# Performance work log

Measured on AMD Instinct MI355X. Metric: run time of the kernel, lower is better.

Reference implementation:

```python
import jax, jax.numpy as jnp
import numpy as np

H = 16      # n_heads
DK = 64     # d_k = d_v = input_dim // n_heads
D = 1024    # input_dim = ouput_dim


def setup_inputs() -> dict:
    key = jax.random.key(0)
    ks = jax.random.split(key, 10)
    s = 1.0 / np.float32(np.sqrt(D))
    inp = {
        'X':  jax.random.normal(ks[0], (2048, D), jnp.float32),
        'X1': jax.random.normal(ks[1], (3072, D), jnp.float32),
        'WQ':  jax.random.normal(ks[2], (D, H * DK), jnp.float32) * s,
        'WK':  jax.random.normal(ks[3], (D, H * DK), jnp.float32) * s,
        'WV':  jax.random.normal(ks[4], (D, H * DK), jnp.float32) * s,
        'WQ1': jax.random.normal(ks[5], (D, H * DK), jnp.float32) * s,
        'WK1': jax.random.normal(ks[6], (D, H * DK), jnp.float32) * s,
        'WV1': jax.random.normal(ks[7], (D, H * DK), jnp.float32) * s,
        'Wfc':  jax.random.normal(ks[8], (H * DK, D), jnp.float32) * s,
        'Wfc1': jax.random.normal(ks[9], (H * DK, D), jnp.float32) * s,
    }
    return inp


def _heads(x):
    # [N, H*DK] -> [H, N, DK]  (matches .view(-1,H,DK).transpose(0,1))
    return x.reshape(-1, H, DK).transpose(1, 0, 2)


def reference(X, X1, WQ, WK, WV, WQ1, WK1, WV1, Wfc, Wfc1):
    scale = jnp.float32(1.0 / np.sqrt(DK))
    Q,  K,  V  = _heads(X @ WQ),  _heads(X @ WK),  _heads(X @ WV)   # [H,N,DK]
    Q1, K1, V1 = _heads(X1 @ WQ1), _heads(X1 @ WK1), _heads(X1 @ WV1)  # [H,N1,DK]

    # direction 1: queries from X1 attend over X
    scores = jnp.einsum('hqd,hkd->hqk', Q1, K) * scale           # [H,N1,N]
    attn = jax.nn.softmax(scores, axis=-1)
    context = jnp.einsum('hqk,hkd->hqd', attn, V)                # [H,N1,DK]

    # direction 2: queries from X attend over X1
    scores1 = jnp.einsum('hqd,hkd->hqk', Q, K1) * scale          # [H,N,N1]
    attn1 = jax.nn.softmax(scores1, axis=-1)
    context1 = jnp.einsum('hqk,hkd->hqd', attn1, V1)             # [H,N,DK]

    # faithful to torch: .transpose(1,2).reshape(-1, H*DK) (head/len axes interleaved)
    context = context.transpose(0, 2, 1).reshape(-1, H * DK)     # [N1, H*DK] rows
    context1 = context1.transpose(0, 2, 1).reshape(-1, H * DK)   # [N,  H*DK] rows

    output = context @ Wfc     # [N1, D]
    output1 = context1 @ Wfc1  # [N,  D]
    return (output, output1)
```

## Files before the change

### kernel.cpp

```cpp
#include <hip/hip_runtime.h>
#include <stdint.h>

typedef unsigned short u16;
typedef unsigned int u32;
typedef u16   u16x4  __attribute__((ext_vector_type(4)));
typedef u16   u16x8  __attribute__((ext_vector_type(8)));
typedef __bf16 bf16x8 __attribute__((ext_vector_type(8)));
typedef float f32x4  __attribute__((ext_vector_type(4)));
typedef u32   u32x2  __attribute__((ext_vector_type(2)));
typedef u32   u32x4  __attribute__((ext_vector_type(4)));

typedef __attribute__((address_space(3))) u16 lds_u16;
typedef __attribute__((address_space(1))) const u16 glb_u16;

static __device__ __forceinline__ u16 f32_bf16(float f) {
    uint32_t u = __builtin_bit_cast(uint32_t, f);
    u += 0x7fffu + ((u >> 16) & 1u);
    return (u16)(u >> 16);
}
static __device__ __forceinline__ u32 pack2(float a, float b) {
#if __has_builtin(__builtin_amdgcn_perm)
    u32 ua = __builtin_bit_cast(u32, a) + 0x8000u;
    u32 ub = __builtin_bit_cast(u32, b) + 0x8000u;
    return __builtin_amdgcn_perm(ub, ua, 0x07060302u);
#else
    return (u32)f32_bf16(a) | ((u32)f32_bf16(b) << 16);
#endif
}
#if __has_builtin(__builtin_amdgcn_exp2f)
#define EXP2(x) __builtin_amdgcn_exp2f(x)
#else
#define EXP2(x) __expf((x) * 0.69314718056f)
#endif
static __device__ __forceinline__ u16x8 cvt8(f32x4 a, f32x4 b) {
    u16x8 v;
#pragma unroll
    for (int e = 0; e < 4; ++e) { v[e] = f32_bf16(a[e]); v[4 + e] = f32_bf16(b[e]); }
    return v;
}

__global__ __launch_bounds__(256) void detect_k(const u16* __restrict__ X, uint32_t* flag) {
    __shared__ int cnt[256];
    int t = threadIdx.x;
    int c = 0;
#pragma unroll
    for (int i = 0; i < 4; ++i) {
        u16 v = X[t + 256 * i];
        int e = (v >> 7) & 0xFF;
        c += (e >= 0xC2) ? 1 : 0;
    }
    cnt[t] = c;
    __syncthreads();
    for (int s = 128; s > 0; s >>= 1) {
        if (t < s) cnt[t] += cnt[t + s];
        __syncthreads();
    }
    if (t == 0) *flag = (cnt[0] > 32) ? 1u : 0u;
}

struct XJob { const void* in; u16* out; int n; };

__global__ __launch_bounds__(256) void convert_x(XJob j0, XJob j1, const uint32_t* __restrict__ flag) {
    const XJob job = (blockIdx.y == 0) ? j0 : j1;
    const bool f32in = (*flag != 0u);
    const int stride = gridDim.x * 256 * 8;
    for (int i = ((int)blockIdx.x * 256 + (int)threadIdx.x) * 8; i < job.n; i += stride) {
        u16x8 v;
        if (f32in) {
            const float* p = (const float*)job.in + i;
            v = cvt8(*(const f32x4*)p, *(const f32x4*)(p + 4));
        } else {
            v = *(const u16x8*)((const u16*)job.in + i);
        }
        *(u16x8*)(job.out + i) = v;
    }
}

struct WJob { const void* in; u16* out; };
struct WBatch8 { WJob j[8]; };

__global__ __launch_bounds__(256) void convert_w(WBatch8 args, const uint32_t* __restrict__ flag) {
    __shared__ u16 tile[64][72];
    const bool f32in = (*flag != 0u);
    const void* in = args.j[blockIdx.z].in;
    u16*       out = args.j[blockIdx.z].out;
    const int t  = threadIdx.x;
    const int r0 = blockIdx.y * 64, c0 = blockIdx.x * 64;
    const int lr = t >> 3, lc = (t & 7) * 8;
#pragma unroll
    for (int pass = 0; pass < 2; ++pass) {
        int r = lr + pass * 32;
        u16x8 v;
        if (f32in) {
            const float* p = (const float*)in + (size_t)(r0 + r) * 1024 + c0 + lc;
            v = cvt8(*(const f32x4*)p, *(const f32x4*)(p + 4));
        } else {
            v = *(const u16x8*)((const u16*)in + (size_t)(r0 + r) * 1024 + c0 + lc);
        }
#pragma unroll
        for (int e = 0; e < 8; ++e) tile[r][lc + e] = v[e];
    }
    __syncthreads();
#pragma unroll
    for (int pass = 0; pass < 2; ++pass) {
        int n = lr + pass * 32;
        u16x8 v;
#pragma unroll
        for (int e = 0; e < 8; ++e) v[e] = tile[lc + e][n];
        *(u16x8*)(out + (size_t)(c0 + n) * 1024 + r0 + lc) = v;
    }
}

struct GemmJob  { const u16* A; const u16* Bt; void* C; int M; int cF32able; int cOffElems; int vtNk; float cScale; };
struct GemmBatch6 { GemmJob j[6]; };

__global__ __launch_bounds__(256) void gemm_bt(GemmBatch6 b, const uint32_t* __restrict__ flag) {
    const GemmJob job = b.j[blockIdx.z];
    const int K = 1024, N = 1024;
    const int m0 = blockIdx.x * 128;
    if (m0 >= job.M) return;
    const int n0 = blockIdx.y * 128;
    const bool cF = job.cF32able && (*flag != 0u);

    __shared__ u16 As[128 * 64];
    __shared__ u16 Bs[128 * 64];

    const int tid  = threadIdx.x;
    const int lane = tid & 63, wave = tid >> 6;
    const int quad = lane >> 4, l16 = lane & 15;
    const int wrow = wave >> 1, wcol = wave & 1;

    f32x4 acc[4][4];
#pragma unroll
    for (int i = 0; i < 4; ++i)
#pragma unroll
        for (int j = 0; j < 4; ++j) acc[i][j] = (f32x4){0.f, 0.f, 0.f, 0.f};

    for (int k0 = 0; k0 < K; k0 += 64) {
        __syncthreads();
#pragma unroll
        for (int i = 0; i < 4; ++i) {
            int id = tid + 256 * i;
            int row = id >> 3, slot = id & 7;
            int src = (slot ^ (row & 7)) * 8;
            __builtin_amdgcn_global_load_lds(
                (glb_u16*)(job.A + (size_t)(m0 + row) * K + k0 + src),
                (lds_u16*)(As + (size_t)id * 8), 16, 0, 0);
            __builtin_amdgcn_global_load_lds(
                (glb_u16*)(job.Bt + (size_t)(n0 + row) * K + k0 + src),
                (lds_u16*)(Bs + (size_t)id * 8), 16, 0, 0);
        }
        __syncthreads();

#pragma unroll
        for (int kc2 = 0; kc2 < 2; ++kc2) {
            bf16x8 af[4], bfb[4];
#pragma unroll
            for (int i = 0; i < 4; ++i) {
                int r  = wrow * 64 + i * 16 + l16;
                af[i]  = *(const bf16x8*)(As + r * 64 + (((kc2 * 4 + quad) ^ (r & 7)) * 8));
                int rn = wcol * 64 + i * 16 + l16;
                bfb[i] = *(const bf16x8*)(Bs + rn * 64 + (((kc2 * 4 + quad) ^ (rn & 7)) * 8));
            }
#pragma unroll
            for (int i = 0; i < 4; ++i)
#pragma unroll
                for (int j = 0; j < 4; ++j)
                    acc[i][j] = __builtin_amdgcn_mfma_f32_16x16x32_bf16(af[i], bfb[j], acc[i][j], 0, 0, 0);
        }
    }

    if (job.vtNk > 0) {
        u16* VT = (u16*)job.C;
        const int Nk2 = job.vtNk;
#pragma unroll
        for (int i = 0; i < 4; ++i)
#pragma unroll
            for (int j = 0; j < 4; ++j) {
                int n   = n0 + wcol * 64 + j * 16 + l16;
                int hh  = n >> 6, dd = n & 63;
                int key = m0 + wrow * 64 + i * 16 + quad * 4;
                int bq  = key & 31;
                int kp  = (key & ~31) | (((bq >> 2) & 3) * 8 + (bq >> 4) * 4);
                u16x4 vv;
#pragma unroll
                for (int r = 0; r < 4; ++r) vv[r] = f32_bf16(acc[i][j][r]);
                *(u16x4*)(VT + (size_t)hh * 64 * Nk2 + (size_t)dd * Nk2 + kp) = vv;
            }
    } else if (cF) {
        float* C = (float*)job.C + job.cOffElems;
#pragma unroll
        for (int i = 0; i < 4; ++i)
#pragma unroll
            for (int j = 0; j < 4; ++j)
#pragma unroll
                for (int r = 0; r < 4; ++r) {
                    int gr = m0 + wrow * 64 + i * 16 + quad * 4 + r;
                    int gc = n0 + wcol * 64 + j * 16 + l16;
                    C[(size_t)gr * N + gc] = acc[i][j][r];
                }
    } else {
        u16* C = (u16*)job.C + job.cOffElems;
        const float cs = job.cScale;
#pragma unroll
        for (int i = 0; i < 4; ++i)
#pragma unroll
            for (int j = 0; j < 4; ++j)
#pragma unroll
                for (int r = 0; r < 4; ++r) {
                    int gr = m0 + wrow * 64 + i * 16 + quad * 4 + r;
                    int gc = n0 + wcol * 64 + j * 16 + l16;
                    C[(size_t)gr * N + gc] = f32_bf16(acc[i][j][r] * cs);
                }
    }
}

struct AttnDir { const u16* Q; const u16* K; const u16* VT; u16* ctxT; int Nq; int Nk; int nBlk; };

__global__ __launch_bounds__(256, 4) void attn_k(AttnDir d0, AttnDir d1) {
    const int D = 1024;
    int b = blockIdx.x;
    const AttnDir dd = (b < d0.nBlk) ? d0 : d1;
    if (blockIdx.x >= (unsigned)d0.nBlk) b -= d0.nBlk;
    const int h  = b & 15;
    const int q0 = (b >> 4) * 64;
    const int Nq = dd.Nq, Nk = dd.Nk;
    const u16* __restrict__ Qp  = dd.Q;
    const u16* __restrict__ Kp  = dd.K;
    const u16* __restrict__ VTp = dd.VT;

    const int tid  = threadIdx.x;
    const int lane = tid & 63, w = tid >> 6;
    const int quad = lane >> 4, l16 = lane & 15;
    const int qhalf = w & 1, khalf = w >> 1;
    const int halfN = Nk >> 1;

    __shared__ u16 smem[18560];
    u16* Ks = smem + w * 4608;
    u16* Vs = Ks + 2048;
    float* Lb = (float*)(smem + 18432);

    bf16x8 aq[2][2];
#pragma unroll
    for (int ms = 0; ms < 2; ++ms)
#pragma unroll
        for (int kc = 0; kc < 2; ++kc) {
            int q = q0 + qhalf * 32 + ms * 16 + l16;
            aq[ms][kc] = *(const bf16x8*)(Qp + (size_t)q * D + h * 64 + kc * 32 + quad * 8);
        }

    f32x4 o[2][4];
#pragma unroll
    for (int ms = 0; ms < 2; ++ms)
#pragma unroll
        for (int nj = 0; nj < 4; ++nj) o[ms][nj] = (f32x4){0.f, 0.f, 0.f, 0.f};
    float rs[2] = {0.f, 0.f};
    const size_t vtBase = (size_t)h * 64 * Nk;
    const int gkBase0 = khalf * halfN;

    int krow[4], ksrc[4], vd[4], vc[4];
#pragma unroll
    for (int i = 0; i < 4; ++i) {
        int id = i * 64 + lane;
        krow[i] = id >> 3;
        ksrc[i] = ((id & 7) ^ (krow[i] & 7)) * 8;
        vd[i]   = id >> 2;
        vc[i]   = id & 3;
    }

    u16x8 kr[4], vr[4];
#pragma unroll
    for (int i = 0; i < 4; ++i) {
        kr[i] = *(const u16x8*)(Kp + (size_t)(gkBase0 + krow[i]) * D + h * 64 + ksrc[i]);
        vr[i] = *(const u16x8*)(VTp + vtBase + (size_t)vd[i] * Nk + gkBase0 + vc[i] * 8);
    }

    for (int k0 = 0; k0 < halfN; k0 += 32) {
#pragma unroll
        for (int i = 0; i < 4; ++i) {
            *(u16x8*)(Ks + (i * 64 + lane) * 8) = kr[i];
            *(u16x8*)(Vs + vd[i] * 40 + vc[i] * 8) = vr[i];
        }
        {
            int kn = (k0 + 32 < halfN) ? (k0 + 32) : 0;
            int gkb = gkBase0 + kn;
#pragma unroll
            for (int i = 0; i < 4; ++i) {
                kr[i] = *(const u16x8*)(Kp + (size_t)(gkb + krow[i]) * D + h * 64 + ksrc[i]);
                vr[i] = *(const u16x8*)(VTp + vtBase + (size_t)vd[i] * Nk + gkb + vc[i] * 8);
            }
        }

        f32x4 s[2][2];
#pragma unroll
        for (int ms = 0; ms < 2; ++ms)
#pragma unroll
            for (int kn = 0; kn < 2; ++kn) s[ms][kn] = (f32x4){0.f, 0.f, 0.f, 0.f};
#pragma unroll
        for (int kn = 0; kn < 2; ++kn)
#pragma unroll
            for (int kc = 0; kc < 2; ++kc) {
                int keyr = kn * 16 + l16;
                int phys = ((kc * 4 + quad) ^ (keyr & 7)) * 8;
                bf16x8 ak = *(const bf16x8*)(Ks + keyr * 64 + phys);
#pragma unroll
                for (int ms = 0; ms < 2; ++ms)
                    s[ms][kn] = __builtin_amdgcn_mfma_f32_16x16x32_bf16(ak, aq[ms][kc], s[ms][kn], 0, 0, 0);
            }

        u32x4 pbf[2];
#pragma unroll
        for (int ms = 0; ms < 2; ++ms) {
#pragma unroll
            for (int kn = 0; kn < 2; ++kn) {
                float p0 = EXP2(s[ms][kn][0]);
                float p1 = EXP2(s[ms][kn][1]);
                float p2 = EXP2(s[ms][kn][2]);
                float p3 = EXP2(s[ms][kn][3]);
                rs[ms] += (p0 + p1) + (p2 + p3);
                pbf[ms][kn * 2 + 0] = pack2(p0, p1);
                pbf[ms][kn * 2 + 1] = pack2(p2, p3);
            }
        }

#pragma unroll
        for (int nj = 0; nj < 4; ++nj) {
            int d = nj * 16 + l16;
            bf16x8 va = *(const bf16x8*)(Vs + d * 40 + quad * 8);
#pragma unroll
            for (int ms = 0; ms < 2; ++ms)
                o[ms][nj] = __builtin_amdgcn_mfma_f32_16x16x32_bf16(
                    va, __builtin_bit_cast(bf16x8, pbf[ms]), o[ms][nj], 0, 0, 0);
        }
    }

#pragma unroll
    for (int ms = 0; ms < 2; ++ms) {
        float v = rs[ms];
        v += __shfl_xor(v, 16, 64);
        v += __shfl_xor(v, 32, 64);
        rs[ms] = v;
    }

    __syncthreads();
    float* Cb = (float*)smem;
    if (khalf == 1) {
#pragma unroll
        for (int ms = 0; ms < 2; ++ms) {
            int ql = qhalf * 32 + ms * 16 + l16;
#pragma unroll
            for (int nj = 0; nj < 4; ++nj)
#pragma unroll
                for (int r = 0; r < 4; ++r)
                    Cb[ql * 65 + nj * 16 + quad * 4 + r] = o[ms][nj][r];
        }
        if (lane < 16) {
#pragma unroll
            for (int ms = 0; ms < 2; ++ms)
                Lb[qhalf * 32 + ms * 16 + l16] = rs[ms];
        }
    }
    __syncthreads();
    if (khalf == 0) {
#pragma unroll
        for (int ms = 0; ms < 2; ++ms) {
            int ql = qhalf * 32 + ms * 16 + l16;
            float inv = 1.0f / (rs[ms] + Lb[ql]);
            int q = q0 + ql;
#pragma unroll
            for (int nj = 0; nj < 4; ++nj)
#pragma unroll
                for (int r = 0; r < 4; ++r) {
                    int d = nj * 16 + quad * 4 + r;
                    float v = (o[ms][nj][r] + Cb[ql * 65 + d]) * inv;
                    dd.ctxT[(size_t)(h * 64 + d) * Nq + q] = f32_bf16(v);
                }
        }
    }
}

extern "C" void kernel_launch(void* const* d_in, const int* in_sizes, int n_in,
                              void* d_out, int out_size, void* d_ws, size_t ws_size,
                              hipStream_t stream) {
    u16* ws = (u16*)d_ws;
    uint32_t* flag = (uint32_t*)ws;
    u16* A = ws + 64;
    const size_t M1 = 1024ull * 1024;
    const float QSC = 0.125f * 1.44269504089f;

    u16* W8   = A;
    u16* Kd1  = A + 8 * M1;
    u16* VT   = A + 10 * M1;
    u16* K1d  = A + 12 * M1;
    u16* VT1  = A + 15 * M1;
    u16* ctx2 = A + 18 * M1;

    u16* outw = (u16*)d_out;
    u16* Q1s  = outw;
    u16* Qs   = outw + 3 * M1;
    u16* Xb   = outw + 5 * M1;
    u16* X1b  = outw + 7 * M1;

    u16* ctx1 = W8;
    u16* WfcT = W8 + 6 * M1;

    detect_k<<<dim3(1), dim3(256), 0, stream>>>((const u16*)d_in[0], flag);

    XJob xj0 = {d_in[0], Xb,  2048 * 1024};
    XJob xj1 = {d_in[1], X1b, 3072 * 1024};
    convert_x<<<dim3(128, 2), dim3(256), 0, stream>>>(xj0, xj1, flag);

    WBatch8 wb;
    for (int i = 0; i < 8; ++i) { wb.j[i].in = d_in[2 + i]; wb.j[i].out = W8 + (size_t)i * M1; }
    convert_w<<<dim3(16, 16, 8), dim3(256), 0, stream>>>(wb, flag);

    GemmBatch6 gp;
    gp.j[0] = (GemmJob){Xb,  W8,          Qs,  2048, 0, 0, 0,    QSC};
    gp.j[1] = (GemmJob){Xb,  W8 + M1,     Kd1, 2048, 0, 0, 0,    1.0f};
    gp.j[2] = (GemmJob){Xb,  W8 + 2 * M1, VT,  2048, 0, 0, 2048, 1.0f};
    gp.j[3] = (GemmJob){X1b, W8 + 3 * M1, Q1s, 3072, 0, 0, 0,    QSC};
    gp.j[4] = (GemmJob){X1b, W8 + 4 * M1, K1d, 3072, 0, 0, 0,    1.0f};
    gp.j[5] = (GemmJob){X1b, W8 + 5 * M1, VT1, 3072, 0, 0, 3072, 1.0f};
    gemm_bt<<<dim3(24, 8, 6), dim3(256), 0, stream>>>(gp, flag);

    AttnDir a0 = {Qs,  K1d, VT1, ctx2, 2048, 3072, 512};
    AttnDir a1 = {Q1s, Kd1, VT,  ctx1, 3072, 2048, 768};
    attn_k<<<dim3(1280), dim3(256), 0, stream>>>(a0, a1);

    GemmBatch6 gf;
    gf.j[0] = (GemmJob){ctx1, WfcT,      d_out, 3072, 1, 0,               0, 1.0f};
    gf.j[1] = (GemmJob){ctx2, WfcT + M1, d_out, 2048, 1, 3 * 1024 * 1024, 0, 1.0f};
    gf.j[2] = gf.j[0]; gf.j[3] = gf.j[0]; gf.j[4] = gf.j[0]; gf.j[5] = gf.j[0];
    gemm_bt<<<dim3(24, 8, 2), dim3(256), 0, stream>>>(gf, flag);
}
```

Baseline: 286.5 us.

## Share K/V tiles across wave pairs via direct global-to-LDS loads

Each pair of waves that shares a key half now loads a single K/V tile into LDS, one wave loading K and the other V^T, using global_load_lds instead of each wave staging its own copy through registers. This cuts LDS use per block from about 37 KB to about 17 KB and raises the occupancy hint from 4 to 6, and it frees the registers that held the prefetched tile. In exchange, the register-level double buffering that overlapped the next tile's load with compute is removed, and two block-wide barriers are added per 32-key step. The V tile row pitch also shrinks from 40 to 32, so padding that may have avoided LDS bank conflicts is gone.

New measurement: 319.6 us. 1.12x slower.

```diff
diff --git a/kernel.cpp b/kernel.cpp
--- a/kernel.cpp
+++ b/kernel.cpp
@@ -217,7 +217,7 @@
 
 struct AttnDir { const u16* Q; const u16* K; const u16* VT; u16* ctxT; int Nq; int Nk; int nBlk; };
 
-__global__ __launch_bounds__(256, 4) void attn_k(AttnDir d0, AttnDir d1) {
+__global__ __launch_bounds__(256, 6) void attn_k(AttnDir d0, AttnDir d1) {
     const int D = 1024;
     int b = blockIdx.x;
     const AttnDir dd = (b < d0.nBlk) ? d0 : d1;
@@ -235,10 +235,10 @@
     const int qhalf = w & 1, khalf = w >> 1;
     const int halfN = Nk >> 1;
 
-    __shared__ u16 smem[18560];
-    u16* Ks = smem + w * 4608;
+    __shared__ u16 smem[8448];
+    u16* Ks = smem + khalf * 4096;
     u16* Vs = Ks + 2048;
-    float* Lb = (float*)(smem + 18432);
+    float* Lb = (float*)(smem + 8320);
 
     bf16x8 aq[2][2];
 #pragma unroll
@@ -255,41 +255,40 @@
 #pragma unroll
         for (int nj = 0; nj < 4; ++nj) o[ms][nj] = (f32x4){0.f, 0.f, 0.f, 0.f};
     float rs[2] = {0.f, 0.f};
-    const size_t vtBase = (size_t)h * 64 * Nk;
     const int gkBase0 = khalf * halfN;
 
-    int krow[4], ksrc[4], vd[4], vc[4];
-#pragma unroll
-    for (int i = 0; i < 4; ++i) {
-        int id = i * 64 + lane;
-        krow[i] = id >> 3;
-        ksrc[i] = ((id & 7) ^ (krow[i] & 7)) * 8;
-        vd[i]   = id >> 2;
-        vc[i]   = id & 3;
-    }
-
-    u16x8 kr[4], vr[4];
-#pragma unroll
-    for (int i = 0; i < 4; ++i) {
-        kr[i] = *(const u16x8*)(Kp + (size_t)(gkBase0 + krow[i]) * D + h * 64 + ksrc[i]);
-        vr[i] = *(const u16x8*)(VTp + vtBase + (size_t)vd[i] * Nk + gkBase0 + vc[i] * 8);
+    const u16* gsrc[4];
+    u16* dstB;
+    size_t kstep;
+    if (qhalf == 0) {
+        dstB = Ks; kstep = (size_t)32 * D;
+#pragma unroll
+        for (int i = 0; i < 4; ++i) {
+            int id  = i * 64 + lane;
+            int row = id >> 3;
+            int src = ((id & 7) ^ (row & 7)) * 8;
+            gsrc[i] = Kp + (size_t)(gkBase0 + row) * D + h * 64 + src;
+        }
+    } else {
+        dstB = Vs; kstep = 32;
+        const size_t vtBase = (size_t)h * 64 * Nk;
+#pragma unroll
+        for (int i = 0; i < 4; ++i) {
+            int id  = i * 64 + lane;
+            gsrc[i] = VTp + vtBase + (size_t)(id >> 2) * Nk + gkBase0 + (id & 3) * 8;
+        }
     }
 
     for (int k0 = 0; k0 < halfN; k0 += 32) {
+        __syncthreads();
 #pragma unroll
         for (int i = 0; i < 4; ++i) {
-            *(u16x8*)(Ks + (i * 64 + lane) * 8) = kr[i];
-            *(u16x8*)(Vs + vd[i] * 40 + vc[i] * 8) = vr[i];
-        }
-        {
-            int kn = (k0 + 32 < halfN) ? (k0 + 32) : 0;
-            int gkb = gkBase0 + kn;
-#pragma unroll
-            for (int i = 0; i < 4; ++i) {
-                kr[i] = *(const u16x8*)(Kp + (size_t)(gkb + krow[i]) * D + h * 64 + ksrc[i]);
-                vr[i] = *(const u16x8*)(VTp + vtBase + (size_t)vd[i] * Nk + gkb + vc[i] * 8);
-            }
-        }
+            __builtin_amdgcn_global_load_lds(
+                (glb_u16*)gsrc[i],
+                (lds_u16*)(dstB + (i * 64 + lane) * 8), 16, 0, 0);
+            gsrc[i] += kstep;
+        }
+        __syncthreads();
 
         f32x4 s[2][2];
 #pragma unroll
@@ -326,7 +325,7 @@
 #pragma unroll
         for (int nj = 0; nj < 4; ++nj) {
             int d = nj * 16 + l16;
-            bf16x8 va = *(const bf16x8*)(Vs + d * 40 + quad * 8);
+            bf16x8 va = *(const bf16x8*)(Vs + d * 32 + quad * 8);
 #pragma unroll
             for (int ms = 0; ms < 2; ++ms)
                 o[ms][nj] = __builtin_amdgcn_mfma_f32_16x16x32_bf16(
```
